# Performance work log

Hardware: AMD Instinct MI355X
Metric: run time of the kernel (lower is better)

## Reference

```python
import jax, jax.numpy as jnp
import numpy as np

B, K2, C, H, W = 8, 9, 1, 256, 1216


def setup_inputs() -> dict:
    key = jax.random.key(0)
    k1, k2 = jax.random.split(key)
    affinity = jax.random.normal(k1, (B, K2, H, W), dtype=jnp.float32)
    feature = jax.random.normal(k2, (B, C, H, W), dtype=jnp.float32)
    return {"affinity": affinity, "feature": feature, "times": 24}


def reference(affinity, feature, times):
    # affinity: [B, 9, H, W]; feature: [B, C, H, W]
    b, k2, h, w = affinity.shape
    a_abs = jnp.abs(affinity)
    a_norm = a_abs / a_abs.sum(axis=1, keepdims=True)  # per-pixel normalized weights [B,9,H,W]

    def step(feat, _):
        fp = jnp.pad(feat, ((0, 0), (0, 0), (1, 1), (1, 1)))  # 3x3 stencil, pad=1
        # Stack the 9 shifted views: [B, 9, C, H, W] (row-major over 3x3 window,
        # matching index = pad_h*3 + pad_w in the torch loop)
        shifts = jnp.stack(
            [fp[:, :, i:i + h, j:j + w] for i in range(3) for j in range(3)],
            axis=1,
        )
        out = jnp.einsum('bncij,bnij->bcij', shifts, a_norm)
        return out, None

    feat, _ = jax.lax.scan(step, feature, None, length=times)
    return feat
```

## Files before the change

### kernel.cpp

```cpp
#include <hip/hip_runtime.h>

#define BB 8
#define HH 256
#define WW 1216
#define TIMES 24

#define KF 4
#define TSZ 26
#define FSZ 34
#define NT 512
#define NFPIX (FSZ*FSZ)
#define TGX 47
#define TGY 10
#define NTILES (TGX*TGY)

#define WPIX 1024
#define WELEM (9*WPIX)
#define WBYTES (WELEM*2)
#define WCHUNKS (WBYTES/256)

static const size_t HW = (size_t)HH * WW;
#define DEQ (1.0f/65535.0f)

typedef float f32x2 __attribute__((ext_vector_type(2)));

#define LDS_BARRIER() do { asm volatile("s_waitcnt lgkmcnt(0)" ::: "memory"); \
                           __builtin_amdgcn_s_barrier(); } while (0)

__device__ __forceinline__ unsigned lds_off(const void* p) {
    return (unsigned)(size_t)(const __attribute__((address_space(3))) void*)p;
}

__device__ __forceinline__ void gload_lds4(const unsigned int* g, void* l) {
    __builtin_amdgcn_global_load_lds(
        (const __attribute__((address_space(1))) void*)g,
        (__attribute__((address_space(3))) void*)l, 4, 0, 0);
}

#define STEPV(BC, o0, o1) do {                                                        \
    unsigned _ab = lds_off((BC) + tb0);                                               \
    f32x2 _v0,_v1,_v2,_v3,_v4,_v5;                                                    \
    asm volatile("ds_read2_b32 %0, %1 offset0:0   offset1:1"  : "=v"(_v0) : "v"(_ab));\
    asm volatile("ds_read2_b32 %0, %1 offset0:2   offset1:34" : "=v"(_v1) : "v"(_ab));\
    asm volatile("ds_read2_b32 %0, %1 offset0:35  offset1:36" : "=v"(_v2) : "v"(_ab));\
    asm volatile("ds_read2_b32 %0, %1 offset0:68  offset1:69" : "=v"(_v3) : "v"(_ab));\
    asm volatile("ds_read2_b32 %0, %1 offset0:70  offset1:102": "=v"(_v4) : "v"(_ab));\
    asm volatile("ds_read2_b32 %0, %1 offset0:103 offset1:104": "=v"(_v5) : "v"(_ab));\
    asm volatile("s_waitcnt lgkmcnt(0)" ::: "memory");                                \
    __builtin_amdgcn_sched_barrier(0);                                                \
    float _t00=_v0.x,_t01=_v0.y,_t02=_v1.x;                                           \
    float _t10=_v1.y,_t11=_v2.x,_t12=_v2.y;                                           \
    float _t20=_v3.x,_t21=_v3.y,_t22=_v4.x;                                           \
    float _t30=_v4.y,_t31=_v5.x,_t32=_v5.y;                                           \
    (o0) = w0[0]*_t00+w0[1]*_t01+w0[2]*_t02 + w0[3]*_t10+w0[4]*_t11+w0[5]*_t12        \
         + w0[6]*_t20+w0[7]*_t21+w0[8]*_t22;                                          \
    (o1) = w1[0]*_t10+w1[1]*_t11+w1[2]*_t12 + w1[3]*_t20+w1[4]*_t21+w1[5]*_t22        \
         + w1[6]*_t30+w1[7]*_t31+w1[8]*_t32;                                          \
} while (0)

#define STORE2(BN) do {                                                               \
    asm volatile("ds_write2_b32 %0, %1, %2 offset0:0 offset1:34"                      \
        :: "v"(lds_off((BN) + cw0)), "v"(r0), "v"(r1) : "memory");                    \
} while (0)

__global__ __launch_bounds__(256) void prep_kernel(const float* __restrict__ aff,
                                                   unsigned short* __restrict__ wq) {
    const int tile = blockIdx.x;
    const int b    = blockIdx.y;
    const int ty   = tile / TGX, tx = tile - ty * TGX;
    const int x0   = tx * TSZ,   y0 = ty * TSZ;
    const float* ap = aff + (size_t)b * 9 * HW;
    unsigned short* op = wq + (size_t)(tile * BB + b) * WELEM;

#pragma unroll
    for (int s = 0; s < 4; ++s) {
        int p  = threadIdx.x + s * 256;
        int wy = p >> 5, wx = p & 31;
        int gy = y0 - (KF - 1) + wy;
        int gx = x0 - (KF - 1) + wx;
        bool in = (unsigned)gy < (unsigned)HH && (unsigned)gx < (unsigned)WW;
        int qi[9];
        if (in) {
            const float* pp = ap + (size_t)gy * WW + gx;
            float v[9], ssum = 0.0f;
#pragma unroll
            for (int n = 0; n < 9; ++n) { v[n] = fabsf(pp[(size_t)n * HW]); ssum += v[n]; }
            float sc = 65535.0f / ssum;
            int tot = 0, m = 0; float vmax = v[0];
#pragma unroll
            for (int n = 0; n < 9; ++n) {
                qi[n] = (int)(v[n] * sc + 0.5f);
                tot += qi[n];
                if (v[n] > vmax) { vmax = v[n]; m = n; }
            }
            int delta = 65535 - tot;
#pragma unroll
            for (int n = 0; n < 9; ++n) qi[n] += (n == m) ? delta : 0;
        } else {
#pragma unroll
            for (int n = 0; n < 9; ++n) qi[n] = 0;
        }
        int pi = ((p >> 6) << 6) + ((p & 31) << 1) + ((p >> 5) & 1);
#pragma unroll
        for (int n = 0; n < 9; ++n) op[n * WPIX + pi] = (unsigned short)qi[n];
    }
}

__global__ __launch_bounds__(NT, 4) void fused4_kernel(const unsigned int* __restrict__ wq,
                                                       const float* __restrict__ src,
                                                       float* __restrict__ dst) {
    __shared__ float S[NFPIX], P[NFPIX], Q[NFPIX];
    __shared__ unsigned int Wl[WELEM / 2];

    const int t    = threadIdx.x;
    const int wv   = t >> 6;
    const int lane = t & 63;
    const int tile = blockIdx.x;
    const int ty   = tile / TGX, tx = tile - ty * TGX;
    const int x0   = tx * TSZ,   y0 = ty * TSZ;

    const int wx  = t & 31;
    const int wy0 = (t >> 5) * 2;
    const int gx  = x0 - (KF - 1) + wx;
    const int gy0 = y0 - (KF - 1) + wy0;
    const int gy1 = gy0 + 1;
    const bool in0 = (unsigned)gy0 < (unsigned)HH && (unsigned)gx < (unsigned)WW;
    const bool in1 = (unsigned)gy1 < (unsigned)HH && (unsigned)gx < (unsigned)WW;
    const int  tb0 = wy0 * FSZ + wx;
    const int  cw0 = (wy0 + 1) * FSZ + (wx + 1);
    const int  widx = (t >> 5) * 32 + (t & 31);

    int foff[3]; bool fok[3];
#pragma unroll
    for (int r = 0; r < 3; ++r) {
        int p  = t + r * NT;
        int fy = p / FSZ, fx = p - fy * FSZ;
        int gfy = y0 - KF + fy, gfx = x0 - KF + fx;
        fok[r]  = (p < NFPIX) && (unsigned)gfy < (unsigned)HH && (unsigned)gfx < (unsigned)WW;
        foff[r] = gfy * WW + gfx;
    }

#pragma unroll
    for (int r = 0; r < 3; ++r) {
        int p = t + r * NT;
        if (p < NFPIX) { P[p] = 0.0f; Q[p] = 0.0f; }
    }

    {
        const unsigned int* w32 = wq + (size_t)(tile * BB) * (WELEM / 2);
        for (int c = wv; c < WCHUNKS; c += 8)
            gload_lds4(w32 + c * 64 + lane, (char*)Wl + c * 256);
    }
#pragma unroll
    for (int r = 0; r < 3; ++r) {
        int p = t + r * NT;
        if (p < NFPIX) S[p] = fok[r] ? src[foff[r]] : 0.0f;
    }
    __syncthreads();

    for (int b = 0; b < BB; ++b) {
        float w0[9], w1[9];
#pragma unroll
        for (int n = 0; n < 9; ++n) {
            unsigned u = Wl[n * (WPIX / 2) + widx];
            w0[n] = (float)(u & 0xffffu) * DEQ;
            w1[n] = (float)(u >> 16)     * DEQ;
        }
        LDS_BARRIER();

        const bool pf = (b + 1 < BB);
        float fn[3];
        if (pf) {
            const unsigned int* w32 = wq + (size_t)(tile * BB + b + 1) * (WELEM / 2);
            for (int c = wv; c < WCHUNKS; c += 8)
                gload_lds4(w32 + c * 64 + lane, (char*)Wl + c * 256);
            const float* sp = src + (size_t)(b + 1) * HW;
#pragma unroll
            for (int r = 0; r < 3; ++r) fn[r] = fok[r] ? sp[foff[r]] : 0.0f;
        }
        __builtin_amdgcn_sched_barrier(0);

        float r0, r1;
        STEPV(S, r0, r1);
        STORE2(P);
        LDS_BARRIER();
        STEPV(P, r0, r1);
        STORE2(Q);
        LDS_BARRIER();
        if (pf) {
#pragma unroll
            for (int r = 0; r < 3; ++r) {
                int p = t + r * NT;
                if (p < NFPIX) S[p] = fn[r];
            }
        }
        STEPV(Q, r0, r1);
        STORE2(P);
        LDS_BARRIER();
        STEPV(P, r0, r1);

        asm volatile("s_waitcnt vmcnt(0)" ::: "memory");
        LDS_BARRIER();

        const size_t base = (size_t)b * HW;
        if ((unsigned)(wx - (KF - 1)) < (unsigned)TSZ) {
            if ((unsigned)(wy0     - (KF - 1)) < (unsigned)TSZ && in0)
                dst[base + (size_t)gy0 * WW + gx] = r0;
            if ((unsigned)(wy0 + 1 - (KF - 1)) < (unsigned)TSZ && in1)
                dst[base + (size_t)gy1 * WW + gx] = r1;
        }
    }
}

extern "C" void kernel_launch(void* const* d_in, const int* in_sizes, int n_in,
                              void* d_out, int out_size, void* d_ws, size_t ws_size,
                              hipStream_t stream) {
    const float* affinity = (const float*)d_in[0];
    const float* feature  = (const float*)d_in[1];

    unsigned short* wq = (unsigned short*)d_ws;
    float* bufA = (float*)((char*)d_ws + (size_t)NTILES * BB * WBYTES);
    float* bufO = (float*)d_out;

    prep_kernel<<<dim3(NTILES, BB), dim3(256), 0, stream>>>(affinity, wq);

    const int NL = TIMES / KF;
    const float* src = feature;
    for (int l = 0; l < NL; ++l) {
        float* dst = (l & 1) ? bufO : bufA;
        fused4_kernel<<<dim3(NTILES), dim3(NT), 0, stream>>>((const unsigned int*)wq, src, dst);
        src = dst;
    }
}
```

Before: 181.0 us.

## Fuse affinity normalization and quantization into first stencil pass

Removes the separate prep kernel. A templated first instance of the fused stencil kernel now reads raw affinity, normalizes and quantizes it to 16-bit per pixel pair, and writes the packed weights to the workspace for later passes while using them directly. The next batch's affinity is prefetched into registers during the stencil steps. This saves a launch and a separate global pass over the affinity, at the cost of extra registers in the first pass, which may cause spills or lower occupancy.

```diff
diff --git a/kernel.cpp b/kernel.cpp
--- a/kernel.cpp
+++ b/kernel.cpp
@@ -63,50 +63,9 @@
         :: "v"(lds_off((BN) + cw0)), "v"(r0), "v"(r1) : "memory");                    \
 } while (0)
 
-__global__ __launch_bounds__(256) void prep_kernel(const float* __restrict__ aff,
-                                                   unsigned short* __restrict__ wq) {
-    const int tile = blockIdx.x;
-    const int b    = blockIdx.y;
-    const int ty   = tile / TGX, tx = tile - ty * TGX;
-    const int x0   = tx * TSZ,   y0 = ty * TSZ;
-    const float* ap = aff + (size_t)b * 9 * HW;
-    unsigned short* op = wq + (size_t)(tile * BB + b) * WELEM;
-
-#pragma unroll
-    for (int s = 0; s < 4; ++s) {
-        int p  = threadIdx.x + s * 256;
-        int wy = p >> 5, wx = p & 31;
-        int gy = y0 - (KF - 1) + wy;
-        int gx = x0 - (KF - 1) + wx;
-        bool in = (unsigned)gy < (unsigned)HH && (unsigned)gx < (unsigned)WW;
-        int qi[9];
-        if (in) {
-            const float* pp = ap + (size_t)gy * WW + gx;
-            float v[9], ssum = 0.0f;
-#pragma unroll
-            for (int n = 0; n < 9; ++n) { v[n] = fabsf(pp[(size_t)n * HW]); ssum += v[n]; }
-            float sc = 65535.0f / ssum;
-            int tot = 0, m = 0; float vmax = v[0];
-#pragma unroll
-            for (int n = 0; n < 9; ++n) {
-                qi[n] = (int)(v[n] * sc + 0.5f);
-                tot += qi[n];
-                if (v[n] > vmax) { vmax = v[n]; m = n; }
-            }
-            int delta = 65535 - tot;
-#pragma unroll
-            for (int n = 0; n < 9; ++n) qi[n] += (n == m) ? delta : 0;
-        } else {
-#pragma unroll
-            for (int n = 0; n < 9; ++n) qi[n] = 0;
-        }
-        int pi = ((p >> 6) << 6) + ((p & 31) << 1) + ((p >> 5) & 1);
-#pragma unroll
-        for (int n = 0; n < 9; ++n) op[n * WPIX + pi] = (unsigned short)qi[n];
-    }
-}
-
-__global__ __launch_bounds__(NT, 4) void fused4_kernel(const unsigned int* __restrict__ wq,
+template <bool FIRST>
+__global__ __launch_bounds__(NT, 4) void fused4_kernel(unsigned int* __restrict__ wq,
+                                                       const float* __restrict__ aff,
                                                        const float* __restrict__ src,
                                                        float* __restrict__ dst) {
     __shared__ float S[NFPIX], P[NFPIX], Q[NFPIX];
@@ -126,6 +85,8 @@
     const int gy1 = gy0 + 1;
     const bool in0 = (unsigned)gy0 < (unsigned)HH && (unsigned)gx < (unsigned)WW;
     const bool in1 = (unsigned)gy1 < (unsigned)HH && (unsigned)gx < (unsigned)WW;
+    const long woff0 = (long)gy0 * WW + gx;
+    const long woff1 = (long)gy1 * WW + gx;
     const int  tb0 = wy0 * FSZ + wx;
     const int  cw0 = (wy0 + 1) * FSZ + (wx + 1);
     const int  widx = (t >> 5) * 32 + (t & 31);
@@ -146,10 +107,17 @@
         if (p < NFPIX) { P[p] = 0.0f; Q[p] = 0.0f; }
     }
 
-    {
+    float a0[9], a1[9];
+    if (!FIRST) {
         const unsigned int* w32 = wq + (size_t)(tile * BB) * (WELEM / 2);
         for (int c = wv; c < WCHUNKS; c += 8)
             gload_lds4(w32 + c * 64 + lane, (char*)Wl + c * 256);
+    } else {
+#pragma unroll
+        for (int n = 0; n < 9; ++n) {
+            a0[n] = in0 ? aff[woff0 + (long)n * (long)HW] : 0.0f;
+            a1[n] = in1 ? aff[woff1 + (long)n * (long)HW] : 0.0f;
+        }
     }
 #pragma unroll
     for (int r = 0; r < 3; ++r) {
@@ -160,20 +128,67 @@
 
     for (int b = 0; b < BB; ++b) {
         float w0[9], w1[9];
-#pragma unroll
-        for (int n = 0; n < 9; ++n) {
-            unsigned u = Wl[n * (WPIX / 2) + widx];
-            w0[n] = (float)(u & 0xffffu) * DEQ;
-            w1[n] = (float)(u >> 16)     * DEQ;
+        if (!FIRST) {
+#pragma unroll
+            for (int n = 0; n < 9; ++n) {
+                unsigned u = Wl[n * (WPIX / 2) + widx];
+                w0[n] = (float)(u & 0xffffu) * DEQ;
+                w1[n] = (float)(u >> 16)     * DEQ;
+            }
+        } else {
+            int qi0[9], qi1[9];
+            {
+                float s0 = 0.0f, s1 = 0.0f;
+#pragma unroll
+                for (int n = 0; n < 9; ++n) {
+                    a0[n] = fabsf(a0[n]); s0 += a0[n];
+                    a1[n] = fabsf(a1[n]); s1 += a1[n];
+                }
+                float sc0 = in0 ? (65535.0f / s0) : 0.0f;
+                float sc1 = in1 ? (65535.0f / s1) : 0.0f;
+                int tot0 = 0, tot1 = 0, m0 = 0, m1 = 0;
+                float vm0 = a0[0], vm1 = a1[0];
+#pragma unroll
+                for (int n = 0; n < 9; ++n) {
+                    qi0[n] = (int)(a0[n] * sc0 + 0.5f); tot0 += qi0[n];
+                    qi1[n] = (int)(a1[n] * sc1 + 0.5f); tot1 += qi1[n];
+                    if (a0[n] > vm0) { vm0 = a0[n]; m0 = n; }
+                    if (a1[n] > vm1) { vm1 = a1[n]; m1 = n; }
+                }
+                int d0 = 65535 - tot0, d1 = 65535 - tot1;
+#pragma unroll
+                for (int n = 0; n < 9; ++n) {
+                    qi0[n] += (in0 && n == m0) ? d0 : 0;
+                    qi1[n] += (in1 && n == m1) ? d1 : 0;
+                }
+            }
+            unsigned int* rec = wq + (size_t)(tile * BB + b) * (WELEM / 2);
+#pragma unroll
+            for (int n = 0; n < 9; ++n) {
+                rec[n * (WPIX / 2) + widx] =
+                    (unsigned)qi0[n] | ((unsigned)qi1[n] << 16);
+                w0[n] = (float)qi0[n] * DEQ;
+                w1[n] = (float)qi1[n] * DEQ;
+            }
         }
         LDS_BARRIER();
 
         const bool pf = (b + 1 < BB);
-        float fn[3];
+        float fn[3], an0[9], an1[9];
         if (pf) {
-            const unsigned int* w32 = wq + (size_t)(tile * BB + b + 1) * (WELEM / 2);
-            for (int c = wv; c < WCHUNKS; c += 8)
-                gload_lds4(w32 + c * 64 + lane, (char*)Wl + c * 256);
+            if (!FIRST) {
+                const unsigned int* w32 =
+                    wq + (size_t)(tile * BB + b + 1) * (WELEM / 2);
+                for (int c = wv; c < WCHUNKS; c += 8)
+                    gload_lds4(w32 + c * 64 + lane, (char*)Wl + c * 256);
+            } else {
+                const float* ap = aff + (size_t)(b + 1) * 9 * HW;
+#pragma unroll
+                for (int n = 0; n < 9; ++n) {
+                    an0[n] = in0 ? ap[woff0 + (long)n * (long)HW] : 0.0f;
+                    an1[n] = in1 ? ap[woff1 + (long)n * (long)HW] : 0.0f;
+                }
+            }
             const float* sp = src + (size_t)(b + 1) * HW;
 #pragma unroll
             for (int r = 0; r < 3; ++r) fn[r] = fok[r] ? sp[foff[r]] : 0.0f;
@@ -198,6 +213,11 @@
         STORE2(P);
         LDS_BARRIER();
         STEPV(P, r0, r1);
+
+        if (FIRST && pf) {
+#pragma unroll
+            for (int n = 0; n < 9; ++n) { a0[n] = an0[n]; a1[n] = an1[n]; }
+        }
 
         asm volatile("s_waitcnt vmcnt(0)" ::: "memory");
         LDS_BARRIER();
@@ -218,17 +238,18 @@
     const float* affinity = (const float*)d_in[0];
     const float* feature  = (const float*)d_in[1];
 
-    unsigned short* wq = (unsigned short*)d_ws;
+    unsigned int* wq = (unsigned int*)d_ws;
     float* bufA = (float*)((char*)d_ws + (size_t)NTILES * BB * WBYTES);
     float* bufO = (float*)d_out;
 
-    prep_kernel<<<dim3(NTILES, BB), dim3(256), 0, stream>>>(affinity, wq);
-
-    const int NL = TIMES / KF;
-    const float* src = feature;
-    for (int l = 0; l < NL; ++l) {
+    fused4_kernel<true><<<dim3(NTILES), dim3(NT), 0, stream>>>(
+        wq, affinity, feature, bufA);
+
+    const float* src = bufA;
+    for (int l = 1; l < TIMES / KF; ++l) {
         float* dst = (l & 1) ? bufO : bufA;
-        fused4_kernel<<<dim3(NTILES), dim3(NT), 0, stream>>>((const unsigned int*)wq, src, dst);
+        fused4_kernel<false><<<dim3(NTILES), dim3(NT), 0, stream>>>(
+            wq, affinity, src, dst);
         src = dst;
     }
 }
```

Measured after the change: 166.9 us. -7.8%, faster.
